# Kernel tuning notes

Hardware: AMD Instinct MI355X
Metric: run time of the kernel (lower is better)

Reference implementation:

```python
import jax, jax.numpy as jnp
import numpy as np

UNIF_T = 2.0
EPS = 1e-12  # matches F.normalize default eps


def _l2norm(a):
    return a / jnp.maximum(jnp.linalg.norm(a, axis=-1, keepdims=True), EPS)


def setup_inputs() -> dict:
    key = jax.random.key(0)
    k1, k2, k3, k4 = jax.random.split(key, 4)
    n, d = 2048, 512
    Q, K = 3, 8192
    n_classes = 16
    x = jax.random.normal(k1, (n, d), dtype=jnp.float32)
    q_data = jax.random.normal(k2, (Q, K, d), dtype=jnp.float32)
    targets = jax.random.randint(k3, (n,), 0, n_classes, dtype=jnp.int64)
    q_targets = jax.random.randint(k4, (Q, K), 0, n_classes, dtype=jnp.int64)
    return {"x": x, "q_data": q_data, "targets": targets, "q_targets": q_targets, "order": 1}


def reference(x, q_data, targets, q_targets, order):
    # x: [n, d], q_data: [Q, K, d], targets: [n], q_targets: [Q, K]
    Q, K, _ = q_data.shape
    xn = _l2norm(x)
    qn = _l2norm(q_data)
    sim = jnp.einsum('nd,qkd->qnk', xn, qn)      # [Q, n, K]
    e = jnp.exp(-UNIF_T * (2.0 - 2.0 * sim))     # [Q, n, K]
    # mask[i, j] = targets[i] == q_targets[order, j]; masked entries of the
    # `order` queue are excluded from that row's mean.
    mask = targets[:, None] == q_targets[order][None, :]   # [n, K] bool
    total = e.sum(axis=(0, 2))                              # [n]
    masked_sum = jnp.where(mask, e[order], 0.0).sum(axis=1) # [n]
    count = (Q * K - mask.sum(axis=1)).astype(e.dtype)      # [n]
    loss = jnp.mean(jnp.log((total - masked_sum) / count))
    return loss
```

## Files before the change

kernel.cpp:

```cpp
#include <hip/hip_runtime.h>
#include <hip/hip_bf16.h>
#include <cstdint>
#include <cstddef>

#define N_ROWS 2048
#define DIM    512
#define QN     3
#define KQ     8192
#define NCOL   (QN * KQ)
#define NCLASS 16

#define BM 128
#define BN 128
#define BK 64
#define NBLK (NCOL / BN)

typedef __attribute__((ext_vector_type(8))) short short8;
typedef __attribute__((ext_vector_type(4))) float f32x4;

__device__ inline unsigned short f2bf(float f) {
    uint32_t u = __float_as_uint(f);
    uint32_t r = (u + 0x7FFFu + ((u >> 16) & 1u)) >> 16;
    return (unsigned short)r;
}

__global__ __launch_bounds__(256) void norm_cast_kernel(
    const float* __restrict__ x, const float* __restrict__ q,
    unsigned short* __restrict__ xb, unsigned short* __restrict__ qb) {
    int row = blockIdx.x * 4 + (threadIdx.x >> 6);
    int lane = threadIdx.x & 63;
    const float* src;
    unsigned short* dst;
    if (row < N_ROWS) {
        src = x + (size_t)row * DIM;
        dst = xb + (size_t)row * DIM;
    } else {
        src = q + (size_t)(row - N_ROWS) * DIM;
        dst = qb + (size_t)(row - N_ROWS) * DIM;
    }
    float4 v0 = ((const float4*)src)[lane * 2];
    float4 v1 = ((const float4*)src)[lane * 2 + 1];
    float ss = v0.x*v0.x + v0.y*v0.y + v0.z*v0.z + v0.w*v0.w
             + v1.x*v1.x + v1.y*v1.y + v1.z*v1.z + v1.w*v1.w;
    #pragma unroll
    for (int off = 1; off < 64; off <<= 1)
        ss += __shfl_xor(ss, off, 64);
    float inv = 1.0f / fmaxf(sqrtf(ss), 1e-12f);
    float vals[8] = {v0.x, v0.y, v0.z, v0.w, v1.x, v1.y, v1.z, v1.w};
    short8 o;
    #pragma unroll
    for (int i = 0; i < 8; i++)
        o[i] = (short)f2bf(vals[i] * inv);
    *(short8*)(dst + lane * 8) = o;
}

__global__ __launch_bounds__(256) void gemm_epilogue_kernel(
    const unsigned short* __restrict__ Xb,
    const unsigned short* __restrict__ Qb,
    const int* __restrict__ targets,
    const int* __restrict__ q_targets,
    const int* __restrict__ order_p,
    float* __restrict__ P) {

    __shared__ unsigned short As[BM * BK];
    __shared__ unsigned short Bs[BN * BK];

    const int tid  = threadIdx.x;
    const int lane = tid & 63;
    const int wave = tid >> 6;
    const int wm = wave >> 1, wn = wave & 1;
    const int quad = lane >> 4;
    const int l15  = lane & 15;
    const int l7   = l15 & 7;

    const int b    = blockIdx.x;
    const int xcd  = b & 7;
    const int g    = b >> 3;
    const int colb = (g >> 4) * 8 + xcd;
    const int rowb = g & 15;
    const int m0 = rowb * BM;
    const int n0 = colb * BN;

    f32x4 acc[4][4];
    #pragma unroll
    for (int i = 0; i < 4; i++)
        #pragma unroll
        for (int j = 0; j < 4; j++)
            acc[i][j] = (f32x4){0.f, 0.f, 0.f, 0.f};

    const int stR = (lane >> 3);
    const int stC = ((lane & 7) ^ stR) * 8;

    for (int k0 = 0; k0 < DIM; k0 += BK) {
        #pragma unroll
        for (int j = 0; j < 4; j++) {
            int chunk = wave * 4 + j;
            int R = chunk * 8 + stR;
            const unsigned short* ga = Xb + (size_t)(m0 + R) * DIM + k0 + stC;
            const unsigned short* gb = Qb + (size_t)(n0 + R) * DIM + k0 + stC;
            __builtin_amdgcn_global_load_lds(
                (const __attribute__((address_space(1))) unsigned int*)ga,
                (__attribute__((address_space(3))) unsigned int*)&As[chunk * 512 + lane * 8],
                16, 0, 0);
            __builtin_amdgcn_global_load_lds(
                (const __attribute__((address_space(1))) unsigned int*)gb,
                (__attribute__((address_space(3))) unsigned int*)&Bs[chunk * 512 + lane * 8],
                16, 0, 0);
        }
        __syncthreads();

        #pragma unroll
        for (int ks = 0; ks < BK; ks += 32) {
            short8 a[4], b2[4];
            #pragma unroll
            for (int mt = 0; mt < 4; mt++)
                a[mt] = *(const short8*)&As[(wm * 64 + mt * 16 + l15) * BK
                                            + ((((ks >> 3) + quad) ^ l7) << 3)];
            #pragma unroll
            for (int nt = 0; nt < 4; nt++)
                b2[nt] = *(const short8*)&Bs[(wn * 64 + nt * 16 + l15) * BK
                                             + ((((ks >> 3) + quad) ^ l7) << 3)];
            #pragma unroll
            for (int mt = 0; mt < 4; mt++)
                #pragma unroll
                for (int nt = 0; nt < 4; nt++)
                    acc[mt][nt] = __builtin_amdgcn_mfma_f32_16x16x32_bf16(
                        a[mt], b2[nt], acc[mt][nt], 0, 0, 0);
        }
        __syncthreads();
    }

    const int ord  = order_p[0];
    const int qIdx = colb / (KQ / BN);
    const bool isOrd = (qIdx == ord);
    const int kbase = n0 - qIdx * KQ;

    int qtv[4] = {0, 0, 0, 0};
    if (isOrd) {
        #pragma unroll
        for (int nt = 0; nt < 4; nt++)
            qtv[nt] = q_targets[ord * KQ + kbase + wn * 64 + nt * 16 + l15];
    }

    float* red = (float*)As;

    #pragma unroll
    for (int mt = 0; mt < 4; mt++) {
        int rowl = wm * 64 + mt * 16 + quad * 4;
        int tg[4] = {0, 0, 0, 0};
        if (isOrd) {
            #pragma unroll
            for (int reg = 0; reg < 4; reg++) tg[reg] = targets[m0 + rowl + reg];
        }
        #pragma unroll
        for (int reg = 0; reg < 4; reg++) {
            float s = 0.f;
            #pragma unroll
            for (int nt = 0; nt < 4; nt++) {
                float sim = acc[mt][nt][reg];
                float e = __expf(4.0f * sim - 4.0f);
                if (isOrd && tg[reg] == qtv[nt]) e = 0.f;
                s += e;
            }
            s += __shfl_xor(s, 1, 64);
            s += __shfl_xor(s, 2, 64);
            s += __shfl_xor(s, 4, 64);
            s += __shfl_xor(s, 8, 64);
            if (l15 == 0)
                red[wn * 128 + rowl + reg] = s;
        }
    }
    __syncthreads();
    if (tid < 128)
        P[(size_t)colb * N_ROWS + m0 + tid] = red[tid] + red[128 + tid];
}

__global__ __launch_bounds__(256) void reduce_kernel(
    const float* __restrict__ P,
    const int* __restrict__ targets,
    const int* __restrict__ q_targets,
    const int* __restrict__ order_p,
    float* __restrict__ out) {
    __shared__ int hist[NCLASS];
    __shared__ float partial[4];
    int tid = threadIdx.x;
    int wave = tid >> 6, lane = tid & 63;
    if (tid < NCLASS) hist[tid] = 0;
    __syncthreads();
    int ord = order_p[0];

    int local[NCLASS];
    #pragma unroll
    for (int c = 0; c < NCLASS; c++) local[c] = 0;
    for (int i = tid; i < KQ; i += 256) {
        int v = q_targets[ord * KQ + i];
        #pragma unroll
        for (int c = 0; c < NCLASS; c++)
            local[c] += __popcll(__ballot(v == c));
    }
    if (lane == 0) {
        #pragma unroll
        for (int c = 0; c < NCLASS; c++)
            atomicAdd(&hist[c], local[c]);
    }
    __syncthreads();

    int r = blockIdx.x * 256 + tid;
    float total = 0.f;
    #pragma unroll 8
    for (int nb = 0; nb < NBLK; nb++)
        total += P[(size_t)nb * N_ROWS + r];
    float cnt = (float)(QN * KQ - hist[targets[r]]);
    float v = logf(total / cnt);

    #pragma unroll
    for (int off = 1; off < 64; off <<= 1)
        v += __shfl_xor(v, off, 64);
    if (lane == 0) partial[wave] = v;
    __syncthreads();
    if (tid == 0)
        atomicAdd(out, (partial[0] + partial[1] + partial[2] + partial[3])
                       * (1.0f / (float)N_ROWS));
}

extern "C" void kernel_launch(void* const* d_in, const int* in_sizes, int n_in,
                              void* d_out, int out_size, void* d_ws, size_t ws_size,
                              hipStream_t stream) {
    const float* x         = (const float*)d_in[0];
    const float* q         = (const float*)d_in[1];
    const int*   targets   = (const int*)d_in[2];
    const int*   q_targets = (const int*)d_in[3];
    const int*   order     = (const int*)d_in[4];
    float* out = (float*)d_out;

    char* ws = (char*)d_ws;
    float* P = (float*)ws;
    unsigned short* Xb = (unsigned short*)(ws + (size_t)NBLK * N_ROWS * 4);
    unsigned short* Qb = Xb + (size_t)N_ROWS * DIM;

    hipMemsetAsync(out, 0, sizeof(float), stream);

    norm_cast_kernel<<<(N_ROWS + NCOL) / 4, 256, 0, stream>>>(x, q, Xb, Qb);

    gemm_epilogue_kernel<<<NBLK * (N_ROWS / BM), 256, 0, stream>>>(
        Xb, Qb, targets, q_targets, order, P);

    reduce_kernel<<<N_ROWS / 256, 256, 0, stream>>>(P, targets, q_targets, order, out);
}
```

Measured before the change: 205.0 us.

## Switch normalized operands and GEMM from bf16 to fp8 MFMA

Normalized rows are scaled by 16 and packed to fp8 instead of bf16. The GEMM loads fp8 tiles with a doubled K-tile and uses the fp8 MFMA, rescaling by 1/256 in the exp epilogue. This halves operand memory traffic and LDS footprint per element and raises MFMA throughput. The cost is lower precision in the similarity values, which feed an exponential before the log-mean loss.

```diff
diff --git a/kernel.cpp b/kernel.cpp
--- a/kernel.cpp
+++ b/kernel.cpp
@@ -12,25 +12,18 @@
 
 #define BM 128
 #define BN 128
-#define BK 64
+#define BK 128
 #define NBLK (NCOL / BN)
 
-typedef __attribute__((ext_vector_type(8))) short short8;
 typedef __attribute__((ext_vector_type(4))) float f32x4;
-
-__device__ inline unsigned short f2bf(float f) {
-    uint32_t u = __float_as_uint(f);
-    uint32_t r = (u + 0x7FFFu + ((u >> 16) & 1u)) >> 16;
-    return (unsigned short)r;
-}
 
 __global__ __launch_bounds__(256) void norm_cast_kernel(
     const float* __restrict__ x, const float* __restrict__ q,
-    unsigned short* __restrict__ xb, unsigned short* __restrict__ qb) {
+    unsigned char* __restrict__ xb, unsigned char* __restrict__ qb) {
     int row = blockIdx.x * 4 + (threadIdx.x >> 6);
     int lane = threadIdx.x & 63;
     const float* src;
-    unsigned short* dst;
+    unsigned char* dst;
     if (row < N_ROWS) {
         src = x + (size_t)row * DIM;
         dst = xb + (size_t)row * DIM;
@@ -45,25 +38,25 @@
     #pragma unroll
     for (int off = 1; off < 64; off <<= 1)
         ss += __shfl_xor(ss, off, 64);
-    float inv = 1.0f / fmaxf(sqrtf(ss), 1e-12f);
-    float vals[8] = {v0.x, v0.y, v0.z, v0.w, v1.x, v1.y, v1.z, v1.w};
-    short8 o;
-    #pragma unroll
-    for (int i = 0; i < 8; i++)
-        o[i] = (short)f2bf(vals[i] * inv);
-    *(short8*)(dst + lane * 8) = o;
+    float inv = 16.0f / fmaxf(sqrtf(ss), 1e-12f);
+    int w0 = __builtin_amdgcn_cvt_pk_fp8_f32(v0.x * inv, v0.y * inv, 0,  false);
+    w0     = __builtin_amdgcn_cvt_pk_fp8_f32(v0.z * inv, v0.w * inv, w0, true);
+    int w1 = __builtin_amdgcn_cvt_pk_fp8_f32(v1.x * inv, v1.y * inv, 0,  false);
+    w1     = __builtin_amdgcn_cvt_pk_fp8_f32(v1.z * inv, v1.w * inv, w1, true);
+    uint2 o; o.x = (unsigned)w0; o.y = (unsigned)w1;
+    *(uint2*)(dst + lane * 8) = o;
 }
 
 __global__ __launch_bounds__(256) void gemm_epilogue_kernel(
-    const unsigned short* __restrict__ Xb,
-    const unsigned short* __restrict__ Qb,
+    const unsigned char* __restrict__ Xb,
+    const unsigned char* __restrict__ Qb,
     const int* __restrict__ targets,
     const int* __restrict__ q_targets,
     const int* __restrict__ order_p,
     float* __restrict__ P) {
 
-    __shared__ unsigned short As[BM * BK];
-    __shared__ unsigned short Bs[BN * BK];
+    __shared__ unsigned char As[BM * BK];
+    __shared__ unsigned char Bs[BN * BK];
 
     const int tid  = threadIdx.x;
     const int lane = tid & 63;
@@ -89,43 +82,43 @@
             acc[i][j] = (f32x4){0.f, 0.f, 0.f, 0.f};
 
     const int stR = (lane >> 3);
-    const int stC = ((lane & 7) ^ stR) * 8;
+    const int stC = ((lane & 7) ^ stR) * 16;
 
     for (int k0 = 0; k0 < DIM; k0 += BK) {
         #pragma unroll
         for (int j = 0; j < 4; j++) {
             int chunk = wave * 4 + j;
             int R = chunk * 8 + stR;
-            const unsigned short* ga = Xb + (size_t)(m0 + R) * DIM + k0 + stC;
-            const unsigned short* gb = Qb + (size_t)(n0 + R) * DIM + k0 + stC;
+            const unsigned char* ga = Xb + (size_t)(m0 + R) * DIM + k0 + stC;
+            const unsigned char* gb = Qb + (size_t)(n0 + R) * DIM + k0 + stC;
             __builtin_amdgcn_global_load_lds(
                 (const __attribute__((address_space(1))) unsigned int*)ga,
-                (__attribute__((address_space(3))) unsigned int*)&As[chunk * 512 + lane * 8],
+                (__attribute__((address_space(3))) unsigned int*)&As[chunk * 1024 + lane * 16],
                 16, 0, 0);
             __builtin_amdgcn_global_load_lds(
                 (const __attribute__((address_space(1))) unsigned int*)gb,
-                (__attribute__((address_space(3))) unsigned int*)&Bs[chunk * 512 + lane * 8],
+                (__attribute__((address_space(3))) unsigned int*)&Bs[chunk * 1024 + lane * 16],
                 16, 0, 0);
         }
         __syncthreads();
 
         #pragma unroll
         for (int ks = 0; ks < BK; ks += 32) {
-            short8 a[4], b2[4];
+            const int c16 = (ks >> 4) + (quad >> 1);
+            const int sw  = ((c16 ^ l7) << 4) + (quad & 1) * 8;
+            long a[4], bb[4];
             #pragma unroll
             for (int mt = 0; mt < 4; mt++)
-                a[mt] = *(const short8*)&As[(wm * 64 + mt * 16 + l15) * BK
-                                            + ((((ks >> 3) + quad) ^ l7) << 3)];
+                a[mt] = *(const long*)&As[(wm * 64 + mt * 16 + l15) * BK + sw];
             #pragma unroll
             for (int nt = 0; nt < 4; nt++)
-                b2[nt] = *(const short8*)&Bs[(wn * 64 + nt * 16 + l15) * BK
-                                             + ((((ks >> 3) + quad) ^ l7) << 3)];
+                bb[nt] = *(const long*)&Bs[(wn * 64 + nt * 16 + l15) * BK + sw];
             #pragma unroll
             for (int mt = 0; mt < 4; mt++)
                 #pragma unroll
                 for (int nt = 0; nt < 4; nt++)
-                    acc[mt][nt] = __builtin_amdgcn_mfma_f32_16x16x32_bf16(
-                        a[mt], b2[nt], acc[mt][nt], 0, 0, 0);
+                    acc[mt][nt] = __builtin_amdgcn_mfma_f32_16x16x32_fp8_fp8(
+                        a[mt], bb[nt], acc[mt][nt], 0, 0, 0);
         }
         __syncthreads();
     }
@@ -157,8 +150,8 @@
             float s = 0.f;
             #pragma unroll
             for (int nt = 0; nt < 4; nt++) {
-                float sim = acc[mt][nt][reg];
-                float e = __expf(4.0f * sim - 4.0f);
+                float v256 = acc[mt][nt][reg];
+                float e = __expf(v256 * 0.015625f - 4.0f);
                 if (isOrd && tg[reg] == qtv[nt]) e = 0.f;
                 s += e;
             }
@@ -235,8 +228,8 @@
 
     char* ws = (char*)d_ws;
     float* P = (float*)ws;
-    unsigned short* Xb = (unsigned short*)(ws + (size_t)NBLK * N_ROWS * 4);
-    unsigned short* Qb = Xb + (size_t)N_ROWS * DIM;
+    unsigned char* Xb = (unsigned char*)(ws + (size_t)NBLK * N_ROWS * 4);
+    unsigned char* Qb = Xb + (size_t)N_ROWS * DIM;
 
     hipMemsetAsync(out, 0, sizeof(float), stream);
 
```

Result: faster. 169.4 us (-17.4%).
